# Kernel optimization log

Hardware: AMD Instinct MI355X
Metric: run time of the kernel (lower is better)

Reference implementation:

```python
import jax, jax.numpy as jnp
import numpy as np

N_NODES, N_EDGES = 50000, 800000
D_H, D_E, HID = 128, 64, 128  # dim_in = D_H + D_E = 192; hidden_dim2 = D_H + HID = 256


def setup_inputs() -> dict:
    key = jax.random.key(0)
    k1, k2, k3, k4, k5 = jax.random.split(key, 5)
    H = jax.random.normal(k1, (N_NODES, D_H), dtype=jnp.float32)
    idx = jax.random.randint(k2, (2, N_EDGES), 0, N_NODES)
    X_e = jax.random.normal(k3, (N_EDGES, D_E), dtype=jnp.float32)
    # kaiming_normal (fan_in mode, relu gain): std = sqrt(2 / fan_in)
    W1 = jax.random.normal(k4, (D_H + D_E, HID), dtype=jnp.float32) * np.sqrt(2.0 / (D_H + D_E)).astype(np.float32)
    W2 = jax.random.normal(k5, (D_H + HID, HID), dtype=jnp.float32) * np.sqrt(2.0 / (D_H + HID)).astype(np.float32)
    return {"H": H, "idx": idx, "X_e": X_e, "W1": W1, "W2": W2}


def reference(H, idx, X_e, W1, W2):
    # gather source-node embeddings and concat with edge features: [E, d_h + d_e]
    x = jnp.concatenate([H[idx[0]], X_e], axis=1)
    y = jax.nn.relu(x @ W1)                                   # [E, HID]
    # scatter_max into destination nodes; empty segments -> 0 (torch_scatter zero fill).
    y = jax.ops.segment_max(y, idx[1], num_segments=H.shape[0])
    y = jnp.maximum(y, 0.0)  # relu output >= 0, so this only fixes -inf empties
    y = jnp.concatenate([H, y], axis=1)                       # [N, d_h + HID]
    y = jax.nn.relu(y @ W2)                                   # [N, HID]
    return y + H  # residual connection (HID == d_h)
```

## Files before the change

kernel.cpp:

```cpp
#include <hip/hip_runtime.h>
#include <hip/hip_bf16.h>
#include <stdint.h>

#define N_NODES 50000
#define N_EDGES 800000
#define D_H 128
#define D_E 64
#define HID 128

#define NODES_PER_BLK 16
#define N_BLOCKS (N_NODES / NODES_PER_BLK)
#define SCAN_B 512
#define N_CHUNKS ((N_NODES + SCAN_B - 1) / SCAN_B)

typedef __attribute__((ext_vector_type(8))) short bf16x8;
typedef __attribute__((ext_vector_type(4))) short s16x4;
typedef __attribute__((ext_vector_type(4))) float f32x4;
typedef __attribute__((ext_vector_type(4))) int i32x4;

__device__ __forceinline__ unsigned short f2bf(float x) {
    unsigned int u = __float_as_uint(x);
    u += 0x7FFFu + ((u >> 16) & 1u);
    return (unsigned short)(u >> 16);
}

__global__ void zero_deg(int* __restrict__ deg) {
    int i = blockIdx.x * blockDim.x + threadIdx.x;
    if (i < N_NODES / 4) ((i32x4*)deg)[i] = i32x4{0, 0, 0, 0};
}

__global__ void hist(const int* __restrict__ idx, int* __restrict__ deg) {
    int i = blockIdx.x * blockDim.x + threadIdx.x;
    atomicAdd(&deg[idx[N_EDGES + i]], 1);
}

__global__ void scan_a(const int* __restrict__ deg, int* __restrict__ sc,
                       int* __restrict__ totals) {
    __shared__ int s[SCAN_B];
    const int tid = threadIdx.x;
    const int i = blockIdx.x * SCAN_B + tid;
    const int v = (i < N_NODES) ? deg[i] : 0;
    s[tid] = v;
    __syncthreads();
    for (int o = 1; o < SCAN_B; o <<= 1) {
        int t = (tid >= o) ? s[tid - o] : 0;
        __syncthreads();
        s[tid] += t;
        __syncthreads();
    }
    if (i < N_NODES) sc[i] = s[tid] - v;
    if (tid == SCAN_B - 1) totals[blockIdx.x] = s[SCAN_B - 1];
}

__global__ void scan_b(int* __restrict__ totals) {
    __shared__ int s[128];
    const int tid = threadIdx.x;
    const int v = (tid < N_CHUNKS) ? totals[tid] : 0;
    s[tid] = v;
    __syncthreads();
    for (int o = 1; o < 128; o <<= 1) {
        int t = (tid >= o) ? s[tid - o] : 0;
        __syncthreads();
        s[tid] += t;
        __syncthreads();
    }
    if (tid < N_CHUNKS) totals[tid] = s[tid] - v;
}

__global__ void scan_c(const int* __restrict__ sc, const int* __restrict__ totals,
                       int* __restrict__ offsets, int* __restrict__ cursor) {
    const int i = blockIdx.x * SCAN_B + threadIdx.x;
    if (i < N_NODES) {
        const int o = sc[i] + totals[blockIdx.x];
        offsets[i] = o;
        cursor[i]  = o;
    }
    if (i == 0) offsets[N_NODES] = N_EDGES;
}

__global__ void scatter(const int* __restrict__ idx, int* __restrict__ cursor,
                        int* __restrict__ perm) {
    int i = blockIdx.x * blockDim.x + threadIdx.x;
    const int d = idx[N_EDGES + i];
    const int p = atomicAdd(&cursor[d], 1);
    perm[p] = i;
}

__global__ __launch_bounds__(256, 2)
void edge_sorted(const float* __restrict__ H,
                 const int* __restrict__ idx,
                 const float* __restrict__ Xe,
                 const float* __restrict__ W1,
                 const int* __restrict__ offsets,
                 const int* __restrict__ perm,
                 unsigned short* __restrict__ gmax) {
    __shared__ unsigned short sX[128][200];
    __shared__ float ymax[17][132];
    __shared__ int sSrc[128];
    __shared__ int sE[128];
    __shared__ unsigned char rowNode[128];
    __shared__ int sOff[NODES_PER_BLK + 1];

    const int tid  = threadIdx.x;
    const int wave = tid >> 6;
    const int lane = tid & 63;
    const int nodeBase = blockIdx.x * NODES_PER_BLK;

    if (tid <= NODES_PER_BLK) sOff[tid] = offsets[nodeBase + tid];
    for (int i = tid; i < 17 * 132; i += 256) ((float*)ymax)[i] = 0.f;

    const int col = lane & 15;
    const int kr0 = (lane >> 4) * 8;
    bf16x8 bfrag[6][2];
    #pragma unroll
    for (int ks = 0; ks < 6; ++ks) {
        #pragma unroll
        for (int nf = 0; nf < 2; ++nf) {
            const int n  = wave * 32 + nf * 16 + col;
            const int kb = ks * 32 + kr0;
            bf16x8 b;
            #pragma unroll
            for (int f = 0; f < 8; ++f) b[f] = (short)f2bf(W1[(kb + f) * HID + n]);
            bfrag[ks][nf] = b;
        }
    }
    __syncthreads();

    const int eBeg = sOff[0];
    const int eEnd = sOff[NODES_PER_BLK];
    const int nE   = eEnd - eBeg;
    const int nTiles = (nE + 127) >> 7;

    const int arow = lane & 15;
    const int rb   = (lane >> 4) * 4;

    for (int t = 0; t < nTiles; ++t) {
        if (tid < 128) {
            const int p = eBeg + t * 128 + tid;
            int e, g;
            if (p < eEnd) {
                e = perm[p];
                g = 0;
                #pragma unroll
                for (int k = 1; k < NODES_PER_BLK; ++k) g += (p >= sOff[k]);
            } else {
                e = perm[eBeg];
                g = NODES_PER_BLK;
            }
            sE[tid] = e;
            sSrc[tid] = idx[e];
            rowNode[tid] = (unsigned char)g;
        }
        __syncthreads();

        #pragma unroll
        for (int it = 0; it < 16; ++it) {
            const int i   = tid + it * 256;
            const int row = i >> 5;
            const int c4  = (i & 31) * 4;
            const f32x4 v = *(const f32x4*)(H + (size_t)sSrc[row] * D_H + c4);
            s16x4 pk = { (short)f2bf(v[0]), (short)f2bf(v[1]),
                         (short)f2bf(v[2]), (short)f2bf(v[3]) };
            *(s16x4*)&sX[row][c4] = pk;
        }
        #pragma unroll
        for (int it = 0; it < 8; ++it) {
            const int i   = tid + it * 256;
            const int row = i >> 4;
            const int c4  = (i & 15) * 4;
            const f32x4 v = *(const f32x4*)(Xe + (size_t)sE[row] * D_E + c4);
            s16x4 pk = { (short)f2bf(v[0]), (short)f2bf(v[1]),
                         (short)f2bf(v[2]), (short)f2bf(v[3]) };
            *(s16x4*)&sX[row][128 + c4] = pk;
        }
        __syncthreads();

        f32x4 acc[8][2];
        #pragma unroll
        for (int m = 0; m < 8; ++m) {
            acc[m][0] = f32x4{0.f, 0.f, 0.f, 0.f};
            acc[m][1] = f32x4{0.f, 0.f, 0.f, 0.f};
        }
        #pragma unroll
        for (int ks = 0; ks < 6; ++ks) {
            #pragma unroll
            for (int m = 0; m < 8; ++m) {
                bf16x8 a = *(const bf16x8*)&sX[m * 16 + arow][ks * 32 + kr0];
                acc[m][0] = __builtin_amdgcn_mfma_f32_16x16x32_bf16(a, bfrag[ks][0], acc[m][0], 0, 0, 0);
                acc[m][1] = __builtin_amdgcn_mfma_f32_16x16x32_bf16(a, bfrag[ks][1], acc[m][1], 0, 0, 0);
            }
        }

        #pragma unroll
        for (int m = 0; m < 8; ++m) {
            #pragma unroll
            for (int r = 0; r < 4; ++r) {
                const int g = rowNode[m * 16 + rb + r];
                const float v0 = acc[m][0][r];
                const float v1 = acc[m][1][r];
                if (g < NODES_PER_BLK) {
                    if (v0 > 0.f) atomicMax((int*)&ymax[g][wave * 32 + col],      __float_as_int(v0));
                    if (v1 > 0.f) atomicMax((int*)&ymax[g][wave * 32 + col + 16], __float_as_int(v1));
                }
            }
        }
        __syncthreads();
    }

    #pragma unroll
    for (int it = 0; it < 2; ++it) {
        const int i  = tid + it * 256;
        const int g  = i >> 5;
        const int c4 = (i & 31) * 4;
        s16x4 pk = { (short)f2bf(ymax[g][c4]),     (short)f2bf(ymax[g][c4 + 1]),
                     (short)f2bf(ymax[g][c4 + 2]), (short)f2bf(ymax[g][c4 + 3]) };
        *(s16x4*)&gmax[(size_t)(nodeBase + g) * HID + c4] = pk;
    }
}

__global__ __launch_bounds__(256, 2)
void node_mlp(const float* __restrict__ H,
              const unsigned short* __restrict__ gmax,
              const float* __restrict__ W2,
              float* __restrict__ out) {
    __shared__ unsigned short sA[64][264];

    const int tid  = threadIdx.x;
    const int wave = tid >> 6;
    const int lane = tid & 63;
    const int base = blockIdx.x * 64;

    const int col = lane & 15;
    const int kr0 = (lane >> 4) * 8;
    bf16x8 bfrag[8][2];
    #pragma unroll
    for (int ks = 0; ks < 8; ++ks) {
        #pragma unroll
        for (int nf = 0; nf < 2; ++nf) {
            const int n  = wave * 32 + nf * 16 + col;
            const int kb = ks * 32 + kr0;
            bf16x8 b;
            #pragma unroll
            for (int f = 0; f < 8; ++f) b[f] = (short)f2bf(W2[(kb + f) * HID + n]);
            bfrag[ks][nf] = b;
        }
    }

    #pragma unroll
    for (int it = 0; it < 8; ++it) {
        const int i   = tid + it * 256;
        const int row = i >> 5;
        const int c4  = (i & 31) * 4;
        int node = base + row;
        if (node >= N_NODES) node = N_NODES - 1;
        const f32x4 v = *(const f32x4*)(H + (size_t)node * D_H + c4);
        s16x4 pk = { (short)f2bf(v[0]), (short)f2bf(v[1]),
                     (short)f2bf(v[2]), (short)f2bf(v[3]) };
        *(s16x4*)&sA[row][c4] = pk;
    }
    #pragma unroll
    for (int it = 0; it < 8; ++it) {
        const int i   = tid + it * 256;
        const int row = i >> 5;
        const int c4  = (i & 31) * 4;
        int node = base + row;
        if (node >= N_NODES) node = N_NODES - 1;
        *(s16x4*)&sA[row][128 + c4] = *(const s16x4*)(gmax + (size_t)node * HID + c4);
    }
    __syncthreads();

    f32x4 acc[4][2];
    #pragma unroll
    for (int m = 0; m < 4; ++m) {
        acc[m][0] = f32x4{0.f, 0.f, 0.f, 0.f};
        acc[m][1] = f32x4{0.f, 0.f, 0.f, 0.f};
    }
    const int arow = lane & 15;
    #pragma unroll
    for (int ks = 0; ks < 8; ++ks) {
        #pragma unroll
        for (int m = 0; m < 4; ++m) {
            bf16x8 a = *(const bf16x8*)&sA[m * 16 + arow][ks * 32 + kr0];
            acc[m][0] = __builtin_amdgcn_mfma_f32_16x16x32_bf16(a, bfrag[ks][0], acc[m][0], 0, 0, 0);
            acc[m][1] = __builtin_amdgcn_mfma_f32_16x16x32_bf16(a, bfrag[ks][1], acc[m][1], 0, 0, 0);
        }
    }

    const int rb = (lane >> 4) * 4;
    #pragma unroll
    for (int m = 0; m < 4; ++m) {
        #pragma unroll
        for (int r = 0; r < 4; ++r) {
            const int node = base + m * 16 + rb + r;
            if (node < N_NODES) {
                const size_t o = (size_t)node * HID + wave * 32 + col;
                out[o]      = fmaxf(acc[m][0][r], 0.f) + H[o];
                out[o + 16] = fmaxf(acc[m][1][r], 0.f) + H[o + 16];
            }
        }
    }
}

extern "C" void kernel_launch(void* const* d_in, const int* in_sizes, int n_in,
                              void* d_out, int out_size, void* d_ws, size_t ws_size,
                              hipStream_t stream) {
    const float* H   = (const float*)d_in[0];
    const int*   idx = (const int*)d_in[1];
    const float* Xe  = (const float*)d_in[2];
    const float* W1  = (const float*)d_in[3];
    const float* W2  = (const float*)d_in[4];
    float* out = (float*)d_out;

    char* ws = (char*)d_ws;
    unsigned short* gmax = (unsigned short*)(ws);
    int* deg     = (int*)(ws + 12800000);
    int* sc      = (int*)(ws + 13000192);
    int* totals  = (int*)(ws + 13200384);
    int* offsets = (int*)(ws + 13200896);
    int* cursor  = (int*)(ws + 13401344);
    int* perm    = (int*)(ws + 13601536);

    zero_deg<<<(N_NODES / 4 + 255) / 256, 256, 0, stream>>>(deg);
    hist<<<N_EDGES / 256, 256, 0, stream>>>(idx, deg);
    scan_a<<<N_CHUNKS, SCAN_B, 0, stream>>>(deg, sc, totals);
    scan_b<<<1, 128, 0, stream>>>(totals);
    scan_c<<<N_CHUNKS, SCAN_B, 0, stream>>>(sc, totals, offsets, cursor);
    scatter<<<N_EDGES / 256, 256, 0, stream>>>(idx, cursor, perm);
    edge_sorted<<<N_BLOCKS, 256, 0, stream>>>(H, idx, Xe, W1, offsets, perm, gmax);
    node_mlp<<<(N_NODES + 63) / 64, 256, 0, stream>>>(H, gmax, W2, out);
}
```

Before: 274.5 us.

## Pre-convert H to bf16, sort source ids, shrink edge tile to 64

Adds a kernel that converts H to bf16 once, so the edge kernel gathers half as many bytes per source row and does no per-edge conversion. The scatter pass now also writes the sorted source indices, which removes a dependent idx lookup. The edge tile drops from 128 to 64 rows, and launch bounds rise to 4 blocks per CU for more occupancy. The max-reduce pre-combines four rows in a register when they belong to the same node, cutting LDS atomics. The bf16 path depends on the workspace being large enough and falls back to the fp32 path otherwise.

```diff
diff --git a/kernel.cpp b/kernel.cpp
--- a/kernel.cpp
+++ b/kernel.cpp
@@ -8,8 +8,9 @@
 #define D_E 64
 #define HID 128
 
-#define NODES_PER_BLK 16
-#define N_BLOCKS (N_NODES / NODES_PER_BLK)
+#define NPB 16
+#define N_BLOCKS (N_NODES / NPB)
+#define MTILE 64
 #define SCAN_B 512
 #define N_CHUNKS ((N_NODES + SCAN_B - 1) / SCAN_B)
 
@@ -22,6 +23,14 @@
     unsigned int u = __float_as_uint(x);
     u += 0x7FFFu + ((u >> 16) & 1u);
     return (unsigned short)(u >> 16);
+}
+
+__global__ void conv_H(const float* __restrict__ H, unsigned short* __restrict__ Hb) {
+    const int i = blockIdx.x * blockDim.x + threadIdx.x;
+    const f32x4 v = ((const f32x4*)H)[i];
+    s16x4 pk = { (short)f2bf(v[0]), (short)f2bf(v[1]),
+                 (short)f2bf(v[2]), (short)f2bf(v[3]) };
+    ((s16x4*)Hb)[i] = pk;
 }
 
 __global__ void zero_deg(int* __restrict__ deg) {
@@ -79,35 +88,38 @@
 }
 
 __global__ void scatter(const int* __restrict__ idx, int* __restrict__ cursor,
-                        int* __restrict__ perm) {
+                        int* __restrict__ perm, int* __restrict__ srcs) {
     int i = blockIdx.x * blockDim.x + threadIdx.x;
+    const int s = idx[i];
     const int d = idx[N_EDGES + i];
     const int p = atomicAdd(&cursor[d], 1);
     perm[p] = i;
-}
-
-__global__ __launch_bounds__(256, 2)
+    srcs[p] = s;
+}
+
+__global__ __launch_bounds__(256, 4)
 void edge_sorted(const float* __restrict__ H,
-                 const int* __restrict__ idx,
+                 const unsigned short* __restrict__ Hb, const int useHb,
                  const float* __restrict__ Xe,
                  const float* __restrict__ W1,
                  const int* __restrict__ offsets,
                  const int* __restrict__ perm,
+                 const int* __restrict__ srcs,
                  unsigned short* __restrict__ gmax) {
-    __shared__ unsigned short sX[128][200];
-    __shared__ float ymax[17][132];
-    __shared__ int sSrc[128];
-    __shared__ int sE[128];
-    __shared__ unsigned char rowNode[128];
-    __shared__ int sOff[NODES_PER_BLK + 1];
+    __shared__ unsigned short sX[MTILE][200];
+    __shared__ float ymax[NPB + 1][132];
+    __shared__ int sSrc[MTILE];
+    __shared__ int sE[MTILE];
+    __shared__ unsigned char rowNode[MTILE];
+    __shared__ int sOff[NPB + 1];
 
     const int tid  = threadIdx.x;
     const int wave = tid >> 6;
     const int lane = tid & 63;
-    const int nodeBase = blockIdx.x * NODES_PER_BLK;
-
-    if (tid <= NODES_PER_BLK) sOff[tid] = offsets[nodeBase + tid];
-    for (int i = tid; i < 17 * 132; i += 256) ((float*)ymax)[i] = 0.f;
+    const int nodeBase = blockIdx.x * NPB;
+
+    if (tid <= NPB) sOff[tid] = offsets[nodeBase + tid];
+    for (int i = tid; i < (NPB + 1) * 132; i += 256) ((float*)ymax)[i] = 0.f;
 
     const int col = lane & 15;
     const int kr0 = (lane >> 4) * 8;
@@ -127,44 +139,53 @@
     __syncthreads();
 
     const int eBeg = sOff[0];
-    const int eEnd = sOff[NODES_PER_BLK];
+    const int eEnd = sOff[NPB];
     const int nE   = eEnd - eBeg;
-    const int nTiles = (nE + 127) >> 7;
+    const int nTiles = (nE + MTILE - 1) / MTILE;
 
     const int arow = lane & 15;
     const int rb   = (lane >> 4) * 4;
+    const int cb   = wave * 32 + col;
 
     for (int t = 0; t < nTiles; ++t) {
-        if (tid < 128) {
-            const int p = eBeg + t * 128 + tid;
-            int e, g;
+        if (tid < MTILE) {
+            const int p  = eBeg + t * MTILE + tid;
+            const int pe = (p < eEnd) ? p : eBeg;
+            int g = NPB;
             if (p < eEnd) {
-                e = perm[p];
                 g = 0;
                 #pragma unroll
-                for (int k = 1; k < NODES_PER_BLK; ++k) g += (p >= sOff[k]);
-            } else {
-                e = perm[eBeg];
-                g = NODES_PER_BLK;
-            }
-            sE[tid] = e;
-            sSrc[tid] = idx[e];
+                for (int k = 1; k < NPB; ++k) g += (p >= sOff[k]);
+            }
+            sE[tid]   = perm[pe];
+            sSrc[tid] = srcs[pe];
             rowNode[tid] = (unsigned char)g;
         }
         __syncthreads();
 
-        #pragma unroll
-        for (int it = 0; it < 16; ++it) {
-            const int i   = tid + it * 256;
-            const int row = i >> 5;
-            const int c4  = (i & 31) * 4;
-            const f32x4 v = *(const f32x4*)(H + (size_t)sSrc[row] * D_H + c4);
-            s16x4 pk = { (short)f2bf(v[0]), (short)f2bf(v[1]),
-                         (short)f2bf(v[2]), (short)f2bf(v[3]) };
-            *(s16x4*)&sX[row][c4] = pk;
-        }
-        #pragma unroll
-        for (int it = 0; it < 8; ++it) {
+        if (useHb) {
+            #pragma unroll
+            for (int it = 0; it < 8; ++it) {
+                const int i   = tid + it * 256;
+                const int row = i >> 5;
+                const int c4  = (i & 31) * 4;
+                *(s16x4*)&sX[row][c4] =
+                    *(const s16x4*)(Hb + (size_t)sSrc[row] * D_H + c4);
+            }
+        } else {
+            #pragma unroll
+            for (int it = 0; it < 8; ++it) {
+                const int i   = tid + it * 256;
+                const int row = i >> 5;
+                const int c4  = (i & 31) * 4;
+                const f32x4 v = *(const f32x4*)(H + (size_t)sSrc[row] * D_H + c4);
+                s16x4 pk = { (short)f2bf(v[0]), (short)f2bf(v[1]),
+                             (short)f2bf(v[2]), (short)f2bf(v[3]) };
+                *(s16x4*)&sX[row][c4] = pk;
+            }
+        }
+        #pragma unroll
+        for (int it = 0; it < 4; ++it) {
             const int i   = tid + it * 256;
             const int row = i >> 4;
             const int c4  = (i & 15) * 4;
@@ -175,16 +196,16 @@
         }
         __syncthreads();
 
-        f32x4 acc[8][2];
-        #pragma unroll
-        for (int m = 0; m < 8; ++m) {
+        f32x4 acc[4][2];
+        #pragma unroll
+        for (int m = 0; m < 4; ++m) {
             acc[m][0] = f32x4{0.f, 0.f, 0.f, 0.f};
             acc[m][1] = f32x4{0.f, 0.f, 0.f, 0.f};
         }
         #pragma unroll
         for (int ks = 0; ks < 6; ++ks) {
             #pragma unroll
-            for (int m = 0; m < 8; ++m) {
+            for (int m = 0; m < 4; ++m) {
                 bf16x8 a = *(const bf16x8*)&sX[m * 16 + arow][ks * 32 + kr0];
                 acc[m][0] = __builtin_amdgcn_mfma_f32_16x16x32_bf16(a, bfrag[ks][0], acc[m][0], 0, 0, 0);
                 acc[m][1] = __builtin_amdgcn_mfma_f32_16x16x32_bf16(a, bfrag[ks][1], acc[m][1], 0, 0, 0);
@@ -192,15 +213,29 @@
         }
 
         #pragma unroll
-        for (int m = 0; m < 8; ++m) {
-            #pragma unroll
-            for (int r = 0; r < 4; ++r) {
-                const int g = rowNode[m * 16 + rb + r];
-                const float v0 = acc[m][0][r];
-                const float v1 = acc[m][1][r];
-                if (g < NODES_PER_BLK) {
-                    if (v0 > 0.f) atomicMax((int*)&ymax[g][wave * 32 + col],      __float_as_int(v0));
-                    if (v1 > 0.f) atomicMax((int*)&ymax[g][wave * 32 + col + 16], __float_as_int(v1));
+        for (int m = 0; m < 4; ++m) {
+            const int r0 = m * 16 + rb;
+            const int g0 = rowNode[r0];
+            const int g3 = rowNode[r0 + 3];
+            if (g0 == g3) {
+                if (g0 < NPB) {
+                    const float v0 = fmaxf(fmaxf(acc[m][0][0], acc[m][0][1]),
+                                           fmaxf(acc[m][0][2], acc[m][0][3]));
+                    const float v1 = fmaxf(fmaxf(acc[m][1][0], acc[m][1][1]),
+                                           fmaxf(acc[m][1][2], acc[m][1][3]));
+                    if (v0 > 0.f) atomicMax((int*)&ymax[g0][cb],      __float_as_int(v0));
+                    if (v1 > 0.f) atomicMax((int*)&ymax[g0][cb + 16], __float_as_int(v1));
+                }
+            } else {
+                #pragma unroll
+                for (int r = 0; r < 4; ++r) {
+                    const int g = rowNode[r0 + r];
+                    if (g < NPB) {
+                        const float v0 = acc[m][0][r];
+                        const float v1 = acc[m][1][r];
+                        if (v0 > 0.f) atomicMax((int*)&ymax[g][cb],      __float_as_int(v0));
+                        if (v1 > 0.f) atomicMax((int*)&ymax[g][cb + 16], __float_as_int(v1));
+                    }
                 }
             }
         }
@@ -218,7 +253,7 @@
     }
 }
 
-__global__ __launch_bounds__(256, 2)
+__global__ __launch_bounds__(256, 4)
 void node_mlp(const float* __restrict__ H,
               const unsigned short* __restrict__ gmax,
               const float* __restrict__ W2,
@@ -319,13 +354,18 @@
     int* offsets = (int*)(ws + 13200896);
     int* cursor  = (int*)(ws + 13401344);
     int* perm    = (int*)(ws + 13601536);
+    int* srcs    = (int*)(ws + 16801536);
+    unsigned short* Hb = (unsigned short*)(ws + 20001536);
+    const int useHb = (ws_size >= (size_t)32801536) ? 1 : 0;
 
     zero_deg<<<(N_NODES / 4 + 255) / 256, 256, 0, stream>>>(deg);
     hist<<<N_EDGES / 256, 256, 0, stream>>>(idx, deg);
+    if (useHb) conv_H<<<N_NODES * D_H / 4 / 256, 256, 0, stream>>>(H, Hb);
     scan_a<<<N_CHUNKS, SCAN_B, 0, stream>>>(deg, sc, totals);
     scan_b<<<1, 128, 0, stream>>>(totals);
     scan_c<<<N_CHUNKS, SCAN_B, 0, stream>>>(sc, totals, offsets, cursor);
-    scatter<<<N_EDGES / 256, 256, 0, stream>>>(idx, cursor, perm);
-    edge_sorted<<<N_BLOCKS, 256, 0, stream>>>(H, idx, Xe, W1, offsets, perm, gmax);
+    scatter<<<N_EDGES / 256, 256, 0, stream>>>(idx, cursor, perm, srcs);
+    edge_sorted<<<N_BLOCKS, 256, 0, stream>>>(H, Hb, useHb, Xe, W1,
+                                              offsets, perm, srcs, gmax);
     node_mlp<<<(N_NODES + 63) / 64, 256, 0, stream>>>(H, gmax, W2, out);
 }
```

New measurement: 308.3 us. 1.12x slower.
